# Kernel tuning notes

Measured on AMD Instinct MI355X. Metric: run time of the kernel, lower is better.

Reference implementation:

```python
import jax, jax.numpy as jnp
import numpy as np

EPS = 0.5          # residual scaling (module __init__ eps)
N = 100_000        # num nodes
E = 1_250_000      # num edges (avg degree ~12.5)
D = 64             # feature dim


def setup_inputs() -> dict:
    key = jax.random.key(0)
    k1, k2, k3 = jax.random.split(key, 3)
    x = jax.random.normal(k1, (N, D), dtype=jnp.float32)
    src = jax.random.randint(k2, (E,), 0, N, dtype=jnp.int32)
    dst = jax.random.randint(k3, (E,), 0, N, dtype=jnp.int32)
    return {"x": x, "src": src, "dst": dst}


def reference(x, src, dst):
    n = x.shape[0]
    # out-degree of each node = number of edges with that node as source
    deg = jax.ops.segment_sum(jnp.ones(src.shape, dtype=x.dtype), src, num_segments=n)
    norm = jnp.power(jnp.maximum(deg, 1.0), -0.5)          # [N]
    edge_norm = norm[src] * norm[dst]                      # [E] (u_mul_v)
    msg = x[src] * edge_norm[:, None]                      # [E, D] (u_mul_e)
    h = jax.ops.segment_sum(msg, dst, num_segments=n)      # sum per destination
    return h + x * EPS
```

## Files before the change

kernel.cpp:

```cpp
#include <hip/hip_runtime.h>

constexpr int D        = 64;
constexpr float EPS    = 0.5f;
constexpr int BKT      = 256;
constexpr int CAPB     = 4096;
constexpr int EPB      = 4096;
constexpr int PTHREADS = 512;
constexpr int EPT      = EPB / PTHREADS;
constexpr int GTHREADS = 512;
constexpr int NBMAX    = 1024;
constexpr int MAXBLK   = 512;

__device__ __forceinline__ unsigned int f2bf(float f) {
    unsigned int u = __float_as_uint(f);
    return (u + 0x7FFFu + ((u >> 16) & 1u)) >> 16;
}
__device__ __forceinline__ float bf2f_lo(unsigned int v) { return __uint_as_float(v << 16); }
__device__ __forceinline__ float bf2f_hi(unsigned int v) { return __uint_as_float(v & 0xFFFF0000u); }


__global__ __launch_bounds__(PTHREADS)
void partition_kernel(const int* __restrict__ src, const int* __restrict__ dst,
                      unsigned int* __restrict__ recB, unsigned char* __restrict__ srecB,
                      unsigned short* __restrict__ tabD, unsigned short* __restrict__ tabS,
                      int E, int NB, int NBP) {
    __shared__ unsigned int  srt[EPB];
    __shared__ unsigned char ssrt[EPB];
    __shared__ int histD[NBMAX];
    __shared__ int histS[NBMAX];
    __shared__ unsigned int rsD[NBMAX];
    __shared__ unsigned int rsS[NBMAX];
    __shared__ unsigned int wsums[PTHREADS / 64];
    __shared__ unsigned int carry;

    const int blk  = blockIdx.x;
    const int base = blk * EPB;
    const int tid  = threadIdx.x;
    const int lane = tid & 63;
    const int wid  = tid >> 6;
    const int cnt  = min(EPB, E - base);
    const bool full = (cnt == EPB);

    for (int b = tid; b < NB; b += PTHREADS) { histD[b] = 0; histS[b] = 0; }
    __syncthreads();

    if (full) {
        const int4* s4 = (const int4*)(src + base);
        const int4* d4 = (const int4*)(dst + base);
        #pragma unroll
        for (int k = 0; k < EPT / 4; ++k) {
            int4 sv = s4[tid + k * PTHREADS];
            int4 dv = d4[tid + k * PTHREADS];
            atomicAdd(&histD[dv.x >> 8], 1); atomicAdd(&histS[sv.x >> 8], 1);
            atomicAdd(&histD[dv.y >> 8], 1); atomicAdd(&histS[sv.y >> 8], 1);
            atomicAdd(&histD[dv.z >> 8], 1); atomicAdd(&histS[sv.z >> 8], 1);
            atomicAdd(&histD[dv.w >> 8], 1); atomicAdd(&histS[sv.w >> 8], 1);
        }
    } else {
        for (int k = 0; k < EPT; ++k) {
            int e = tid + k * PTHREADS;
            if (e < cnt) {
                atomicAdd(&histD[dst[base + e] >> 8], 1);
                atomicAdd(&histS[src[base + e] >> 8], 1);
            }
        }
    }
    __syncthreads();

    if (tid == 0) carry = 0;
    __syncthreads();
    for (int bp = 0; bp < NB; bp += PTHREADS) {
        int idx = bp + tid;
        unsigned int orig = (idx < NB) ? (unsigned int)histD[idx] : 0u;
        if (idx < NB) histD[idx] = 0;
        unsigned int v = orig;
        #pragma unroll
        for (int off = 1; off < 64; off <<= 1) {
            unsigned int t = __shfl_up(v, off);
            if (lane >= off) v += t;
        }
        if (lane == 63) wsums[wid] = v;
        __syncthreads();
        unsigned int add = carry;
        for (int w = 0; w < wid; ++w) add += wsums[w];
        if (idx < NB) rsD[idx] = v - orig + add;
        __syncthreads();
        if (tid == 0) {
            unsigned int s = carry;
            for (int w = 0; w < PTHREADS / 64; ++w) s += wsums[w];
            carry = s;
        }
        __syncthreads();
    }
    if (tid == 0) carry = 0;
    __syncthreads();
    for (int bp = 0; bp < NB; bp += PTHREADS) {
        int idx = bp + tid;
        unsigned int orig = (idx < NB) ? (unsigned int)histS[idx] : 0u;
        if (idx < NB) histS[idx] = 0;
        unsigned int v = orig;
        #pragma unroll
        for (int off = 1; off < 64; off <<= 1) {
            unsigned int t = __shfl_up(v, off);
            if (lane >= off) v += t;
        }
        if (lane == 63) wsums[wid] = v;
        __syncthreads();
        unsigned int add = carry;
        for (int w = 0; w < wid; ++w) add += wsums[w];
        if (idx < NB) rsS[idx] = v - orig + add;
        __syncthreads();
        if (tid == 0) {
            unsigned int s = carry;
            for (int w = 0; w < PTHREADS / 64; ++w) s += wsums[w];
            carry = s;
        }
        __syncthreads();
    }

    for (int b = tid; b <= NB; b += PTHREADS) {
        unsigned short vD = (unsigned short)((b < NB) ? rsD[b] : (unsigned int)cnt);
        unsigned short vS = (unsigned short)((b < NB) ? rsS[b] : (unsigned int)cnt);
        tabD[(size_t)blk * NBP + b] = vD;
        tabS[(size_t)blk * NBP + b] = vS;
    }

    if (full) {
        const int4* s4 = (const int4*)(src + base);
        const int4* d4 = (const int4*)(dst + base);
        #pragma unroll
        for (int k = 0; k < EPT / 4; ++k) {
            int4 sv = s4[tid + k * PTHREADS];
            int4 dv = d4[tid + k * PTHREADS];
            int ss[4] = {sv.x, sv.y, sv.z, sv.w};
            int tt[4] = {dv.x, dv.y, dv.z, dv.w};
            #pragma unroll
            for (int j = 0; j < 4; ++j) {
                int s = ss[j], t = tt[j];
                int bD = t >> 8;
                int r  = atomicAdd(&histD[bD], 1);
                srt[rsD[bD] + r] = ((unsigned int)s << 8) | (unsigned int)(t & (BKT - 1));
                int bS = s >> 8;
                int r2 = atomicAdd(&histS[bS], 1);
                ssrt[rsS[bS] + r2] = (unsigned char)(s & (BKT - 1));
            }
        }
    } else {
        for (int k = 0; k < EPT; ++k) {
            int e = tid + k * PTHREADS;
            if (e < cnt) {
                int s = src[base + e], t = dst[base + e];
                int bD = t >> 8;
                int r  = atomicAdd(&histD[bD], 1);
                srt[rsD[bD] + r] = ((unsigned int)s << 8) | (unsigned int)(t & (BKT - 1));
                int bS = s >> 8;
                int r2 = atomicAdd(&histS[bS], 1);
                ssrt[rsS[bS] + r2] = (unsigned char)(s & (BKT - 1));
            }
        }
    }
    __syncthreads();

    {
        uint4* go = (uint4*)(recB + (size_t)blk * EPB);
        const uint4* gi = (const uint4*)srt;
        for (int i = tid; i < EPB / 4; i += PTHREADS) go[i] = gi[i];
        uint4* so = (uint4*)(srecB + (size_t)blk * EPB);
        const uint4* si = (const uint4*)ssrt;
        for (int i = tid; i < EPB / 16; i += PTHREADS) so[i] = si[i];
    }
}

__global__ __launch_bounds__(256)
void normyh_kernel(const unsigned char* __restrict__ srecB, const unsigned short* __restrict__ tabS,
                   const float2* __restrict__ x2, unsigned int* __restrict__ yh,
                   float* __restrict__ norm, int n, int NBLK, int NBP) {
    const int b   = blockIdx.x;
    const int tid = threadIdx.x;
    __shared__ int hist[BKT];
    __shared__ float nrm[BKT];
    hist[tid] = 0;
    __syncthreads();
    const int g  = tid >> 4;
    const int gl = tid & 15;
    for (int blk = g; blk < NBLK; blk += 16) {
        int o0 = tabS[(size_t)blk * NBP + b];
        int o1 = tabS[(size_t)blk * NBP + b + 1];
        const unsigned char* p = srecB + (size_t)blk * EPB;
        for (int j = o0 + gl; j < o1; j += 16) atomicAdd(&hist[p[j]], 1);
    }
    __syncthreads();
    int node = b * BKT + tid;
    float nm = rsqrtf(fmaxf((float)hist[tid], 1.0f));
    nrm[tid] = nm;
    if (node < n) norm[node] = nm;
    __syncthreads();
    int nodes = n - b * BKT;
    if (nodes > BKT) nodes = BKT;
    if (nodes < 0) nodes = 0;
    int total = nodes * (D / 2);
    size_t gbase = (size_t)b * BKT * (D / 2);
    for (int i = tid; i < total; i += 256) {
        float2 v = x2[gbase + i];
        float nm2 = nrm[i >> 5];
        yh[gbase + i] = f2bf(v.x * nm2) | (f2bf(v.y * nm2) << 16);
    }
}

__global__ __launch_bounds__(GTHREADS)
void sortgather_kernel(const unsigned int* __restrict__ recB, const unsigned short* __restrict__ tabD,
                       const float* __restrict__ norm, const uint4* __restrict__ yr4,
                       const float4* __restrict__ x4, float4* __restrict__ out4,
                       int n, int NBLK, int NBP) {
    __shared__ unsigned int recs[CAPB];
    __shared__ unsigned int srcs[CAPB];
    __shared__ unsigned short segoff[MAXBLK];
    __shared__ unsigned int dstoff[MAXBLK + 1];
    __shared__ int hist[BKT];
    __shared__ int rankb[BKT];
    __shared__ int rsL[BKT];
    __shared__ float nrmL[BKT];
    __shared__ unsigned int wsums[GTHREADS / 64];
    __shared__ unsigned int carry;
    const int b    = blockIdx.x;
    const int tid  = threadIdx.x;
    const int lane = tid & 63;
    const int wid  = tid >> 6;

    for (int blk = tid; blk < NBLK; blk += GTHREADS) {
        unsigned int o0 = tabD[(size_t)blk * NBP + b];
        unsigned int o1 = tabD[(size_t)blk * NBP + b + 1];
        segoff[blk] = (unsigned short)o0;
        dstoff[blk] = o1 - o0;
    }
    if (tid < BKT) {
        int node = b * BKT + tid;
        nrmL[tid] = (node < n) ? norm[node] : 1.0f;
    }
    if (tid == 0) carry = 0;
    __syncthreads();
    for (int bp = 0; bp < NBLK; bp += GTHREADS) {
        int idx = bp + tid;
        unsigned int orig = (idx < NBLK) ? dstoff[idx] : 0u;
        unsigned int v = orig;
        #pragma unroll
        for (int off = 1; off < 64; off <<= 1) {
            unsigned int t = __shfl_up(v, off);
            if (lane >= off) v += t;
        }
        if (lane == 63) wsums[wid] = v;
        __syncthreads();
        unsigned int add = carry;
        for (int w = 0; w < wid; ++w) add += wsums[w];
        if (idx < NBLK) dstoff[idx] = v - orig + add;
        __syncthreads();
        if (tid == 0) {
            unsigned int s = carry;
            for (int w = 0; w < GTHREADS / 64; ++w) s += wsums[w];
            carry = s;
        }
        __syncthreads();
    }
    if (tid == 0) dstoff[NBLK] = carry;
    __syncthreads();
    const int cnt = (int)dstoff[NBLK];
    const int nch = (cnt > CAPB) ? (cnt + CAPB - 1) / CAPB : 1;

    const int fl  = lane & 7;
    const int oct = lane >> 3;

    for (int c = 0; c < nch; ++c) {
        const unsigned int lo = (unsigned int)c * CAPB;
        const unsigned int hi = min((unsigned int)cnt, lo + (unsigned int)CAPB);
        const int wlen = (int)(hi - lo);
        {
            const int g  = tid >> 4;
            const int gl = tid & 15;
            for (int blk = g; blk < NBLK; blk += GTHREADS / 16) {
                unsigned int dbase = dstoff[blk], dend = dstoff[blk + 1];
                unsigned int s0 = max(dbase, lo), s1 = min(dend, hi);
                if (s0 < s1) {
                    size_t glo = (size_t)blk * EPB + segoff[blk] + (s0 - dbase);
                    for (unsigned int j = gl; j < s1 - s0; j += 16)
                        recs[s0 - lo + j] = recB[glo + j];
                }
            }
        }
        __syncthreads();
        if (tid < BKT) hist[tid] = 0;
        __syncthreads();
        for (int i = tid; i < wlen; i += GTHREADS) atomicAdd(&hist[recs[i] & (BKT - 1)], 1);
        __syncthreads();
        {
            int v = (tid < BKT) ? hist[tid] : 0;
            #pragma unroll
            for (int off = 1; off < 64; off <<= 1) {
                int t = __shfl_up(v, off);
                if (lane >= off) v += t;
            }
            if (tid < BKT && lane == 63) wsums[wid] = (unsigned int)v;
            __syncthreads();
            if (tid < BKT) {
                int add = 0;
                for (int w = 0; w < wid; ++w) add += (int)wsums[w];
                int excl = v + add - hist[tid];
                rankb[tid] = excl;
                rsL[tid]   = excl;
            }
        }
        __syncthreads();
        for (int i = tid; i < wlen; i += GTHREADS) {
            unsigned int v = recs[i];
            int pos = atomicAdd(&rankb[v & (BKT - 1)], 1);
            srcs[pos] = v >> 8;
        }
        __syncthreads();

        #pragma unroll
        for (int r = 0; r < BKT / 64; ++r) {
            int ln   = r * 64 + wid * 8 + oct;
            int node = b * BKT + ln;
            bool valid = node < n;
            int rsl = valid ? rsL[ln]  : 0;
            int cl  = valid ? hist[ln] : 0;
            int m = cl;
            m = max(m, __shfl_xor(m, 8));
            m = max(m, __shfl_xor(m, 16));
            m = max(m, __shfl_xor(m, 32));
            float a0 = 0.f, a1 = 0.f, a2 = 0.f, a3 = 0.f;
            float a4 = 0.f, a5 = 0.f, a6 = 0.f, a7 = 0.f;
            for (int k = 0; k < m; k += 8) {
                int sb[8];
                #pragma unroll
                for (int j = 0; j < 8; ++j) {
                    int kj = k + j;
                    sb[j] = (kj < cl) ? (int)srcs[rsl + kj] : -1;
                }
                #pragma unroll
                for (int j = 0; j < 8; ++j) {
                    bool take = sb[j] >= 0;
                    int s = take ? sb[j] : 0;
                    uint4 v = yr4[(size_t)s * 8 + fl];
                    if (!take) { v.x = 0u; v.y = 0u; v.z = 0u; v.w = 0u; }
                    a0 += bf2f_lo(v.x); a1 += bf2f_hi(v.x);
                    a2 += bf2f_lo(v.y); a3 += bf2f_hi(v.y);
                    a4 += bf2f_lo(v.z); a5 += bf2f_hi(v.z);
                    a6 += bf2f_lo(v.w); a7 += bf2f_hi(v.w);
                }
            }
            if (valid) {
                float nt = nrmL[ln];
                size_t basei = (size_t)node * 16 + fl * 2;
                float4 r0, r1;
                if (c == 0) {
                    float4 xv0 = x4[basei], xv1 = x4[basei + 1];
                    r0.x = a0 * nt + EPS * xv0.x;  r0.y = a1 * nt + EPS * xv0.y;
                    r0.z = a2 * nt + EPS * xv0.z;  r0.w = a3 * nt + EPS * xv0.w;
                    r1.x = a4 * nt + EPS * xv1.x;  r1.y = a5 * nt + EPS * xv1.y;
                    r1.z = a6 * nt + EPS * xv1.z;  r1.w = a7 * nt + EPS * xv1.w;
                } else {
                    float4 p0 = out4[basei], p1 = out4[basei + 1];
                    r0.x = p0.x + a0 * nt;  r0.y = p0.y + a1 * nt;
                    r0.z = p0.z + a2 * nt;  r0.w = p0.w + a3 * nt;
                    r1.x = p1.x + a4 * nt;  r1.y = p1.y + a5 * nt;
                    r1.z = p1.z + a6 * nt;  r1.w = p1.w + a7 * nt;
                }
                out4[basei] = r0;
                out4[basei + 1] = r1;
            }
        }
    }
}


__global__ void fb_hist(const int* __restrict__ src, int* __restrict__ deg, int E) {
    int e = blockIdx.x * blockDim.x + threadIdx.x;
    if (e < E) atomicAdd(&deg[src[e]], 1);
}
__global__ void fb_norm(const int* __restrict__ deg, float* __restrict__ norm, int n) {
    int i = blockIdx.x * blockDim.x + threadIdx.x;
    if (i < n) norm[i] = rsqrtf(fmaxf((float)deg[i], 1.0f));
}
__global__ void fb_init_out(const float4* __restrict__ x, float4* __restrict__ out, int n4) {
    int i = blockIdx.x * blockDim.x + threadIdx.x;
    if (i < n4) {
        float4 v = x[i];
        out[i] = make_float4(v.x * EPS, v.y * EPS, v.z * EPS, v.w * EPS);
    }
}
__global__ void fb_scatter(const float* __restrict__ x, const int* __restrict__ src,
                           const int* __restrict__ dst, const float* __restrict__ norm,
                           float* __restrict__ out, int E) {
    long long tid = (long long)blockIdx.x * blockDim.x + threadIdx.x;
    int e = (int)(tid >> 6), d = (int)(tid & 63);
    if (e < E) {
        int s = src[e], t = dst[e];
        atomicAdd(&out[(size_t)t * D + d], norm[s] * norm[t] * x[(size_t)s * D + d]);
    }
}


extern "C" void kernel_launch(void* const* d_in, const int* in_sizes, int n_in,
                              void* d_out, int out_size, void* d_ws, size_t ws_size,
                              hipStream_t stream) {
    const float* x   = (const float*)d_in[0];
    const int*   src = (const int*)d_in[1];
    const int*   dst = (const int*)d_in[2];
    float* out = (float*)d_out;

    const int ND = in_sizes[0];
    const int E  = in_sizes[1];
    const int n  = ND / D;
    const int NB   = (n + BKT - 1) / BKT;
    const int NBLK = (E + EPB - 1) / EPB;
    const int NBP  = NB + 1;
    constexpr int B = 256;

    size_t off = 0;
    auto take = [&](size_t bytes) { size_t o = off; off = (off + bytes + 15) & ~15ull; return o; };
    size_t o_rec  = take((size_t)NBLK * EPB * 4);
    size_t o_srec = take((size_t)NBLK * EPB);
    size_t o_tabD = take((size_t)NBLK * NBP * 2);
    size_t o_tabS = take((size_t)NBLK * NBP * 2);
    size_t o_yh   = take((size_t)ND * 2);
    size_t o_norm = take((size_t)n * 4);
    size_t need = off;

    if (NB <= NBMAX && NBLK <= MAXBLK && n < (1 << 24) && need <= ws_size && E > 0) {
        char* ws = (char*)d_ws;
        unsigned int*   recB  = (unsigned int*)(ws + o_rec);
        unsigned char*  srecB = (unsigned char*)(ws + o_srec);
        unsigned short* tabD  = (unsigned short*)(ws + o_tabD);
        unsigned short* tabS  = (unsigned short*)(ws + o_tabS);
        unsigned int*   yh    = (unsigned int*)(ws + o_yh);
        float*          norm  = (float*)(ws + o_norm);

        partition_kernel<<<NBLK, PTHREADS, 0, stream>>>(src, dst, recB, srecB,
                                                        tabD, tabS, E, NB, NBP);
        normyh_kernel<<<NB, B, 0, stream>>>(srecB, tabS, (const float2*)x, yh, norm,
                                            n, NBLK, NBP);
        sortgather_kernel<<<NB, GTHREADS, 0, stream>>>(recB, tabD, norm, (const uint4*)yh,
                                                       (const float4*)x, (float4*)out,
                                                       n, NBLK, NBP);
    } else {
        int*   deg  = (int*)d_ws;
        float* norm = (float*)d_ws + n;
        hipMemsetAsync(deg, 0, (size_t)n * sizeof(int), stream);
        fb_hist<<<(E + B - 1) / B, B, 0, stream>>>(src, deg, E);
        fb_norm<<<(n + B - 1) / B, B, 0, stream>>>(deg, norm, n);
        fb_init_out<<<(ND / 4 + B - 1) / B, B, 0, stream>>>((const float4*)x, (float4*)out, ND / 4);
        long long total = (long long)E * D;
        fb_scatter<<<(int)((total + B - 1) / B), B, 0, stream>>>(x, src, dst, norm, out, E);
    }
}
```

Measured before the change: 166.5 us.

## Pack dst/src histograms, widen normyh block, split sortgather buckets across two blocks

The partition kernel now packs the destination and source bucket counts into one 32-bit shared word (low/high 16 bits), so a single prefix scan replaces two and the shared footprint shrinks. normyh runs with 512 threads, stages per-block segment offsets in shared memory, and uses 8-lane groups for the degree histogram. sortgather launches twice as many blocks, each handling half of a 256-node bucket, to raise parallelism. The cost is that both halves re-read the same bucket records and filter them, doubling that read traffic. NBMAX also drops to 512, which tightens the limit for taking the fast path.

```diff
diff --git a/kernel.cpp b/kernel.cpp
--- a/kernel.cpp
+++ b/kernel.cpp
@@ -3,12 +3,14 @@
 constexpr int D        = 64;
 constexpr float EPS    = 0.5f;
 constexpr int BKT      = 256;
+constexpr int HBKT     = 128;
 constexpr int CAPB     = 4096;
 constexpr int EPB      = 4096;
 constexpr int PTHREADS = 512;
 constexpr int EPT      = EPB / PTHREADS;
 constexpr int GTHREADS = 512;
-constexpr int NBMAX    = 1024;
+constexpr int NTHREADS = 512;
+constexpr int NBMAX    = 512;
 constexpr int MAXBLK   = 512;
 
 __device__ __forceinline__ unsigned int f2bf(float f) {
@@ -26,10 +28,8 @@
                       int E, int NB, int NBP) {
     __shared__ unsigned int  srt[EPB];
     __shared__ unsigned char ssrt[EPB];
-    __shared__ int histD[NBMAX];
-    __shared__ int histS[NBMAX];
-    __shared__ unsigned int rsD[NBMAX];
-    __shared__ unsigned int rsS[NBMAX];
+    __shared__ unsigned int histDS[NBMAX];
+    __shared__ unsigned int rsDS[NBMAX];
     __shared__ unsigned int wsums[PTHREADS / 64];
     __shared__ unsigned int carry;
 
@@ -41,7 +41,7 @@
     const int cnt  = min(EPB, E - base);
     const bool full = (cnt == EPB);
 
-    for (int b = tid; b < NB; b += PTHREADS) { histD[b] = 0; histS[b] = 0; }
+    for (int b = tid; b < NB; b += PTHREADS) histDS[b] = 0;
     __syncthreads();
 
     if (full) {
@@ -51,17 +51,17 @@
         for (int k = 0; k < EPT / 4; ++k) {
             int4 sv = s4[tid + k * PTHREADS];
             int4 dv = d4[tid + k * PTHREADS];
-            atomicAdd(&histD[dv.x >> 8], 1); atomicAdd(&histS[sv.x >> 8], 1);
-            atomicAdd(&histD[dv.y >> 8], 1); atomicAdd(&histS[sv.y >> 8], 1);
-            atomicAdd(&histD[dv.z >> 8], 1); atomicAdd(&histS[sv.z >> 8], 1);
-            atomicAdd(&histD[dv.w >> 8], 1); atomicAdd(&histS[sv.w >> 8], 1);
+            atomicAdd(&histDS[dv.x >> 8], 1u); atomicAdd(&histDS[sv.x >> 8], 0x10000u);
+            atomicAdd(&histDS[dv.y >> 8], 1u); atomicAdd(&histDS[sv.y >> 8], 0x10000u);
+            atomicAdd(&histDS[dv.z >> 8], 1u); atomicAdd(&histDS[sv.z >> 8], 0x10000u);
+            atomicAdd(&histDS[dv.w >> 8], 1u); atomicAdd(&histDS[sv.w >> 8], 0x10000u);
         }
     } else {
         for (int k = 0; k < EPT; ++k) {
             int e = tid + k * PTHREADS;
             if (e < cnt) {
-                atomicAdd(&histD[dst[base + e] >> 8], 1);
-                atomicAdd(&histS[src[base + e] >> 8], 1);
+                atomicAdd(&histDS[dst[base + e] >> 8], 1u);
+                atomicAdd(&histDS[src[base + e] >> 8], 0x10000u);
             }
         }
     }
@@ -71,8 +71,8 @@
     __syncthreads();
     for (int bp = 0; bp < NB; bp += PTHREADS) {
         int idx = bp + tid;
-        unsigned int orig = (idx < NB) ? (unsigned int)histD[idx] : 0u;
-        if (idx < NB) histD[idx] = 0;
+        unsigned int orig = (idx < NB) ? histDS[idx] : 0u;
+        if (idx < NB) histDS[idx] = 0;
         unsigned int v = orig;
         #pragma unroll
         for (int off = 1; off < 64; off <<= 1) {
@@ -83,7 +83,7 @@
         __syncthreads();
         unsigned int add = carry;
         for (int w = 0; w < wid; ++w) add += wsums[w];
-        if (idx < NB) rsD[idx] = v - orig + add;
+        if (idx < NB) rsDS[idx] = v - orig + add;
         __syncthreads();
         if (tid == 0) {
             unsigned int s = carry;
@@ -92,37 +92,11 @@
         }
         __syncthreads();
     }
-    if (tid == 0) carry = 0;
-    __syncthreads();
-    for (int bp = 0; bp < NB; bp += PTHREADS) {
-        int idx = bp + tid;
-        unsigned int orig = (idx < NB) ? (unsigned int)histS[idx] : 0u;
-        if (idx < NB) histS[idx] = 0;
-        unsigned int v = orig;
-        #pragma unroll
-        for (int off = 1; off < 64; off <<= 1) {
-            unsigned int t = __shfl_up(v, off);
-            if (lane >= off) v += t;
-        }
-        if (lane == 63) wsums[wid] = v;
-        __syncthreads();
-        unsigned int add = carry;
-        for (int w = 0; w < wid; ++w) add += wsums[w];
-        if (idx < NB) rsS[idx] = v - orig + add;
-        __syncthreads();
-        if (tid == 0) {
-            unsigned int s = carry;
-            for (int w = 0; w < PTHREADS / 64; ++w) s += wsums[w];
-            carry = s;
-        }
-        __syncthreads();
-    }
 
     for (int b = tid; b <= NB; b += PTHREADS) {
-        unsigned short vD = (unsigned short)((b < NB) ? rsD[b] : (unsigned int)cnt);
-        unsigned short vS = (unsigned short)((b < NB) ? rsS[b] : (unsigned int)cnt);
-        tabD[(size_t)blk * NBP + b] = vD;
-        tabS[(size_t)blk * NBP + b] = vS;
+        unsigned int v = (b < NB) ? rsDS[b] : ((unsigned int)cnt | ((unsigned int)cnt << 16));
+        tabD[(size_t)blk * NBP + b] = (unsigned short)(v & 0xFFFFu);
+        tabS[(size_t)blk * NBP + b] = (unsigned short)(v >> 16);
     }
 
     if (full) {
@@ -138,11 +112,11 @@
             for (int j = 0; j < 4; ++j) {
                 int s = ss[j], t = tt[j];
                 int bD = t >> 8;
-                int r  = atomicAdd(&histD[bD], 1);
-                srt[rsD[bD] + r] = ((unsigned int)s << 8) | (unsigned int)(t & (BKT - 1));
+                unsigned int r = atomicAdd(&histDS[bD], 1u) & 0xFFFFu;
+                srt[(rsDS[bD] & 0xFFFFu) + r] = ((unsigned int)s << 8) | (unsigned int)(t & (BKT - 1));
                 int bS = s >> 8;
-                int r2 = atomicAdd(&histS[bS], 1);
-                ssrt[rsS[bS] + r2] = (unsigned char)(s & (BKT - 1));
+                unsigned int r2 = atomicAdd(&histDS[bS], 0x10000u) >> 16;
+                ssrt[(rsDS[bS] >> 16) + r2] = (unsigned char)(s & (BKT - 1));
             }
         }
     } else {
@@ -151,11 +125,11 @@
             if (e < cnt) {
                 int s = src[base + e], t = dst[base + e];
                 int bD = t >> 8;
-                int r  = atomicAdd(&histD[bD], 1);
-                srt[rsD[bD] + r] = ((unsigned int)s << 8) | (unsigned int)(t & (BKT - 1));
+                unsigned int r = atomicAdd(&histDS[bD], 1u) & 0xFFFFu;
+                srt[(rsDS[bD] & 0xFFFFu) + r] = ((unsigned int)s << 8) | (unsigned int)(t & (BKT - 1));
                 int bS = s >> 8;
-                int r2 = atomicAdd(&histS[bS], 1);
-                ssrt[rsS[bS] + r2] = (unsigned char)(s & (BKT - 1));
+                unsigned int r2 = atomicAdd(&histDS[bS], 0x10000u) >> 16;
+                ssrt[(rsDS[bS] >> 16) + r2] = (unsigned char)(s & (BKT - 1));
             }
         }
     }
@@ -171,36 +145,44 @@
     }
 }
 
-__global__ __launch_bounds__(256)
+__global__ __launch_bounds__(NTHREADS)
 void normyh_kernel(const unsigned char* __restrict__ srecB, const unsigned short* __restrict__ tabS,
                    const float2* __restrict__ x2, unsigned int* __restrict__ yh,
                    float* __restrict__ norm, int n, int NBLK, int NBP) {
     const int b   = blockIdx.x;
     const int tid = threadIdx.x;
+    __shared__ unsigned int segO[MAXBLK];
     __shared__ int hist[BKT];
     __shared__ float nrm[BKT];
-    hist[tid] = 0;
-    __syncthreads();
-    const int g  = tid >> 4;
-    const int gl = tid & 15;
-    for (int blk = g; blk < NBLK; blk += 16) {
-        int o0 = tabS[(size_t)blk * NBP + b];
-        int o1 = tabS[(size_t)blk * NBP + b + 1];
+    if (tid < BKT) hist[tid] = 0;
+    for (int blk = tid; blk < NBLK; blk += NTHREADS) {
+        unsigned int o0 = tabS[(size_t)blk * NBP + b];
+        unsigned int o1 = tabS[(size_t)blk * NBP + b + 1];
+        segO[blk] = o0 | (o1 << 16);
+    }
+    __syncthreads();
+    const int g  = tid >> 3;
+    const int gl = tid & 7;
+    for (int blk = g; blk < NBLK; blk += NTHREADS / 8) {
+        unsigned int u = segO[blk];
+        int o0 = (int)(u & 0xFFFFu), o1 = (int)(u >> 16);
         const unsigned char* p = srecB + (size_t)blk * EPB;
-        for (int j = o0 + gl; j < o1; j += 16) atomicAdd(&hist[p[j]], 1);
-    }
-    __syncthreads();
-    int node = b * BKT + tid;
-    float nm = rsqrtf(fmaxf((float)hist[tid], 1.0f));
-    nrm[tid] = nm;
-    if (node < n) norm[node] = nm;
+        for (int j = o0 + gl; j < o1; j += 8) atomicAdd(&hist[p[j]], 1);
+    }
+    __syncthreads();
+    if (tid < BKT) {
+        int node = b * BKT + tid;
+        float nm = rsqrtf(fmaxf((float)hist[tid], 1.0f));
+        nrm[tid] = nm;
+        if (node < n) norm[node] = nm;
+    }
     __syncthreads();
     int nodes = n - b * BKT;
     if (nodes > BKT) nodes = BKT;
     if (nodes < 0) nodes = 0;
     int total = nodes * (D / 2);
     size_t gbase = (size_t)b * BKT * (D / 2);
-    for (int i = tid; i < total; i += 256) {
+    for (int i = tid; i < total; i += NTHREADS) {
         float2 v = x2[gbase + i];
         float nm2 = nrm[i >> 5];
         yh[gbase + i] = f2bf(v.x * nm2) | (f2bf(v.y * nm2) << 16);
@@ -216,16 +198,18 @@
     __shared__ unsigned int srcs[CAPB];
     __shared__ unsigned short segoff[MAXBLK];
     __shared__ unsigned int dstoff[MAXBLK + 1];
-    __shared__ int hist[BKT];
-    __shared__ int rankb[BKT];
-    __shared__ int rsL[BKT];
-    __shared__ float nrmL[BKT];
+    __shared__ int hist[HBKT];
+    __shared__ int rankb[HBKT];
+    __shared__ int rsL[HBKT];
+    __shared__ float nrmL[HBKT];
     __shared__ unsigned int wsums[GTHREADS / 64];
     __shared__ unsigned int carry;
-    const int b    = blockIdx.x;
-    const int tid  = threadIdx.x;
-    const int lane = tid & 63;
-    const int wid  = tid >> 6;
+    const int b     = blockIdx.x >> 1;
+    const int half  = blockIdx.x & 1;
+    const int hbase = half * HBKT;
+    const int tid   = threadIdx.x;
+    const int lane  = tid & 63;
+    const int wid   = tid >> 6;
 
     for (int blk = tid; blk < NBLK; blk += GTHREADS) {
         unsigned int o0 = tabD[(size_t)blk * NBP + b];
@@ -233,8 +217,8 @@
         segoff[blk] = (unsigned short)o0;
         dstoff[blk] = o1 - o0;
     }
-    if (tid < BKT) {
-        int node = b * BKT + tid;
+    if (tid < HBKT) {
+        int node = b * BKT + hbase + tid;
         nrmL[tid] = (node < n) ? norm[node] : 1.0f;
     }
     if (tid == 0) carry = 0;
@@ -274,35 +258,37 @@
         const unsigned int hi = min((unsigned int)cnt, lo + (unsigned int)CAPB);
         const int wlen = (int)(hi - lo);
         {
-            const int g  = tid >> 4;
-            const int gl = tid & 15;
-            for (int blk = g; blk < NBLK; blk += GTHREADS / 16) {
+            const int cg  = tid >> 4;
+            const int cgl = tid & 15;
+            for (int blk = cg; blk < NBLK; blk += GTHREADS / 16) {
                 unsigned int dbase = dstoff[blk], dend = dstoff[blk + 1];
                 unsigned int s0 = max(dbase, lo), s1 = min(dend, hi);
                 if (s0 < s1) {
                     size_t glo = (size_t)blk * EPB + segoff[blk] + (s0 - dbase);
-                    for (unsigned int j = gl; j < s1 - s0; j += 16)
+                    for (unsigned int j = cgl; j < s1 - s0; j += 16)
                         recs[s0 - lo + j] = recB[glo + j];
                 }
             }
         }
         __syncthreads();
-        if (tid < BKT) hist[tid] = 0;
-        __syncthreads();
-        for (int i = tid; i < wlen; i += GTHREADS) atomicAdd(&hist[recs[i] & (BKT - 1)], 1);
+        if (tid < HBKT) hist[tid] = 0;
+        __syncthreads();
+        for (int i = tid; i < wlen; i += GTHREADS) {
+            int ln = (int)(recs[i] & (BKT - 1));
+            if ((ln >> 7) == half) atomicAdd(&hist[ln & (HBKT - 1)], 1);
+        }
         __syncthreads();
         {
-            int v = (tid < BKT) ? hist[tid] : 0;
+            int v = (tid < HBKT) ? hist[tid] : 0;
             #pragma unroll
             for (int off = 1; off < 64; off <<= 1) {
                 int t = __shfl_up(v, off);
                 if (lane >= off) v += t;
             }
-            if (tid < BKT && lane == 63) wsums[wid] = (unsigned int)v;
+            if (tid < HBKT && lane == 63) wsums[wid] = (unsigned int)v;
             __syncthreads();
-            if (tid < BKT) {
-                int add = 0;
-                for (int w = 0; w < wid; ++w) add += (int)wsums[w];
+            if (tid < HBKT) {
+                int add = (wid == 1) ? (int)wsums[0] : 0;
                 int excl = v + add - hist[tid];
                 rankb[tid] = excl;
                 rsL[tid]   = excl;
@@ -311,15 +297,18 @@
         __syncthreads();
         for (int i = tid; i < wlen; i += GTHREADS) {
             unsigned int v = recs[i];
-            int pos = atomicAdd(&rankb[v & (BKT - 1)], 1);
-            srcs[pos] = v >> 8;
+            int ln = (int)(v & (BKT - 1));
+            if ((ln >> 7) == half) {
+                int pos = atomicAdd(&rankb[ln & (HBKT - 1)], 1);
+                srcs[pos] = v >> 8;
+            }
         }
         __syncthreads();
 
         #pragma unroll
-        for (int r = 0; r < BKT / 64; ++r) {
+        for (int r = 0; r < HBKT / 64; ++r) {
             int ln   = r * 64 + wid * 8 + oct;
-            int node = b * BKT + ln;
+            int node = b * BKT + hbase + ln;
             bool valid = node < n;
             int rsl = valid ? rsL[ln]  : 0;
             int cl  = valid ? hist[ln] : 0;
@@ -437,11 +426,11 @@
 
         partition_kernel<<<NBLK, PTHREADS, 0, stream>>>(src, dst, recB, srecB,
                                                         tabD, tabS, E, NB, NBP);
-        normyh_kernel<<<NB, B, 0, stream>>>(srecB, tabS, (const float2*)x, yh, norm,
-                                            n, NBLK, NBP);
-        sortgather_kernel<<<NB, GTHREADS, 0, stream>>>(recB, tabD, norm, (const uint4*)yh,
-                                                       (const float4*)x, (float4*)out,
-                                                       n, NBLK, NBP);
+        normyh_kernel<<<NB, NTHREADS, 0, stream>>>(srecB, tabS, (const float2*)x, yh, norm,
+                                                   n, NBLK, NBP);
+        sortgather_kernel<<<2 * NB, GTHREADS, 0, stream>>>(recB, tabD, norm, (const uint4*)yh,
+                                                           (const float4*)x, (float4*)out,
+                                                           n, NBLK, NBP);
     } else {
         int*   deg  = (int*)d_ws;
         float* norm = (float*)d_ws + n;
```

Result: slower. 169.9 us (+2.0%).
